# Kernel tuning notes

Hardware: AMD Instinct MI355X
Metric: run time of the kernel (lower is better)

## Reference

```python
import jax, jax.numpy as jnp
import numpy as np

N, D1, D2, B = 8, 2048, 1024, 512
D = D1 * D2
MAXBW = 3
NUM_PART = 5          # num_possible_partitions
TEMP = 0.01           # TEMPERATURE used in df_lt
DENOS = (3.0, 5.0, 17.0)  # 2^2-1, 2^2+1, 2^4+1


def ste_floor(x):
    # straight-through floor: forward floor, backward identity
    return x + jax.lax.stop_gradient(jnp.floor(x) - x)


def segmented_mean(piece, scheme, msp):
    """Replicates the inner python scan over sorted rows.
    piece:  (N, D) sorted residual errors
    scheme: (N-1, D) rounded split decisions (0/1), per column
    msp:    (N-1, D) soft split probabilities (grad factors), per column
    Returns (N, D): each row gets grad_ * (segment mean) of its segment.
    """
    n = piece.shape[0]
    buf = jnp.zeros_like(piece[0])
    cnt = jnp.zeros_like(piece[0])
    g = jnp.ones_like(piece[0])
    reset = jnp.zeros(piece.shape[1], dtype=bool)
    vlist, blist = [], []
    for i in range(n):
        buf = jnp.where(reset, piece[i], buf + piece[i])
        cnt = jnp.where(reset, 1.0, cnt + 1.0)
        g = jnp.where(reset, 1.0, g)
        if i == n - 1:
            vlist.append(g * (buf / cnt))
            blist.append(jnp.ones_like(reset))
        else:
            b = scheme[i] > 0.5
            vlist.append(jnp.where(b, g * msp[i], 0.0) * (buf / cnt))
            blist.append(b)
            g = jnp.where(b, g, g * (1.0 - msp[i]))
            reset = b
    # broadcast each segment-end value back to all rows of its segment
    out = vlist[-1]
    outs = [out]
    for i in range(n - 2, -1, -1):
        out = jnp.where(blist[i], vlist[i], out)
        outs.append(out)
    return jnp.stack(outs[::-1], axis=0)


def residual_quant(U, vsum, s, thr):
    """One residual quantization level (the update_partition=True branch)."""
    res = U - vsum                                   # (N, D)
    idx_maps = jnp.argsort(res, axis=0)              # torch.sort ascending, dim=0
    sorted_err = jnp.take_along_axis(res, idx_maps, axis=0)
    delta = sorted_err[1:] - sorted_err[:-1]         # (N-1, D), >= 0
    delta = delta / jnp.max(delta)
    msp = jax.nn.sigmoid((delta - thr) / TEMP)       # mean_split_point (N-1, D)
    rs = jnp.round(msp)                              # round_split, 0/1

    nm1 = N - 1
    P = 2 ** nm1  # all possible split-column patterns (torch.unique over dim=1)
    weights = (2 ** jnp.arange(nm1 - 1, -1, -1)).astype(jnp.int32)  # row 0 = MSB (lexicographic)
    code = jnp.sum(rs.astype(jnp.int32) * weights[:, None], axis=0)  # (D,)
    counts = jnp.zeros((P,), jnp.int32).at[code].add(1)
    present = counts > 0
    # torch.unique sorts patterns lexicographically -> rank = #present codes below
    rank_of_code = jnp.cumsum(present.astype(jnp.int32)) - present.astype(jnp.int32)
    order = jnp.argsort(-counts)                     # codes by count descending
    top_codes = order[:NUM_PART]
    top_ranks = rank_of_code[top_codes]              # s_indices[:NUM_PART]
    # binary patterns for every possible code
    patterns = ((jnp.arange(P)[:, None] >> jnp.arange(nm1 - 1, -1, -1)[None, :]) & 1).astype(jnp.float32)  # (P, N-1)
    inter = patterns @ patterns[top_codes].T         # (P, NUM_PART)
    sel = jnp.argmax(inter, axis=1)
    reassigned = top_ranks[sel]                      # (P,)
    is_top = jnp.any(rank_of_code[:, None] == top_ranks[None, :], axis=1)
    final_rank = jnp.where(is_top, rank_of_code, reassigned)  # (P,)
    c_rank = final_rank[code]                        # clustered_indices, (D,)

    # NOTE: original indexes round_split / mean_split_point columns BY the
    # unique-cluster index value s_idx (a quirk of the source); replicate it.
    scheme_used = rs[:, c_rank]                      # (N-1, D)
    msp_used = msp[:, c_rank]                        # (N-1, D)

    inner = segmented_mean(sorted_err, scheme_used, msp_used)  # (N, D)
    # einsum('cb,cba->ab', inner, one_hot(idx_maps)) == unsort along dim 0
    inv = jnp.argsort(idx_maps, axis=0)
    grouped = jnp.take_along_axis(inner, inv, axis=0)
    return s * ste_floor(grouped / s)


def setup_inputs():
    key = jax.random.key(0)
    k1, k2 = jax.random.split(key)
    x = jax.random.normal(k1, (B, N, D1), dtype=jnp.float32)
    # kaiming_normal_ on (N, D): std = sqrt(2 / fan_in), fan_in = D
    U = jax.random.normal(k2, (N, D), dtype=jnp.float32) * np.float32(np.sqrt(2.0 / D))
    thres_mean = jnp.full((D2,), -1.3, dtype=jnp.float32)
    return {"x": x, "U": U, "thres_mean": thres_mean}


def reference(x, U, thres_mean):
    beta = jnp.max(U)
    alpha = jnp.min(U)
    s = (beta - alpha) / DENOS[0]
    vsum = s * ste_floor(U / s)                      # base quantization level
    thr = jax.nn.sigmoid(jnp.repeat(thres_mean, D1))  # thres_mean.repeat_interleave(D1)
    for deno in DENOS[1:MAXBW]:
        s = s / deno
        vsum = vsum + residual_quant(U, vsum, s, thr)
    w = vsum.reshape(N, D1, D2)
    return jnp.einsum('bnd,ndl->bnl', x, w)
```

## Files before the change

### kernel.cpp

```cpp
#include <hip/hip_runtime.h>
#include <hip/hip_bf16.h>
#include <math.h>

#define NROW 8
#define DT   2097152
#define DD1  2048
#define DD2  1024
#define BATCH 512
#define NBLK 2048
#define NCH  4


typedef __attribute__((ext_vector_type(8))) short short8;
typedef __attribute__((ext_vector_type(4))) float f32x4;

__device__ __forceinline__ unsigned fenc(float f){
  unsigned u = __float_as_uint(f);
  return (u & 0x80000000u) ? ~u : (u | 0x80000000u);
}
__device__ __forceinline__ float fdec(unsigned k){
  return (k & 0x80000000u) ? __uint_as_float(k ^ 0x80000000u) : __uint_as_float(~k);
}
__device__ __forceinline__ float sigmoid_ref(float z){
  #pragma clang fp contract(off)
  return 1.0f / (1.0f + expf(-z));
}
__device__ __forceinline__ unsigned short f2bf(float f){
  __hip_bfloat16 h = __float2bfloat16(f);
  return *reinterpret_cast<unsigned short*>(&h);
}

#define CSWAPV(a,b) { float _lo=fminf(a,b), _hi=fmaxf(a,b); a=_lo; b=_hi; }
__device__ __forceinline__ void sort8v(float v[8]){
  CSWAPV(v[0],v[1]) CSWAPV(v[2],v[3]) CSWAPV(v[4],v[5]) CSWAPV(v[6],v[7])
  CSWAPV(v[0],v[2]) CSWAPV(v[1],v[3]) CSWAPV(v[4],v[6]) CSWAPV(v[5],v[7])
  CSWAPV(v[1],v[2]) CSWAPV(v[5],v[6])
  CSWAPV(v[0],v[4]) CSWAPV(v[1],v[5]) CSWAPV(v[2],v[6]) CSWAPV(v[3],v[7])
  CSWAPV(v[2],v[4]) CSWAPV(v[3],v[5])
  CSWAPV(v[1],v[2]) CSWAPV(v[3],v[4]) CSWAPV(v[5],v[6])
}
__device__ __forceinline__ void cswapkv(float&av,int&ai,float&bv,int&bi){
  bool sw = (av > bv) || ((av == bv) && (ai > bi));
  float nav = sw ? bv : av; float nbv = sw ? av : bv;
  int   nai = sw ? bi : ai; int   nbi = sw ? ai : bi;
  av = nav; bv = nbv; ai = nai; bi = nbi;
}
#define CSWAPK(i,j) cswapkv(v[i],ix[i],v[j],ix[j]);
__device__ __forceinline__ void sort8kv(float v[8], int ix[8]){
  CSWAPK(0,1) CSWAPK(2,3) CSWAPK(4,5) CSWAPK(6,7)
  CSWAPK(0,2) CSWAPK(1,3) CSWAPK(4,6) CSWAPK(5,7)
  CSWAPK(1,2) CSWAPK(5,6)
  CSWAPK(0,4) CSWAPK(1,5) CSWAPK(2,6) CSWAPK(3,7)
  CSWAPK(2,4) CSWAPK(3,5)
  CSWAPK(1,2) CSWAPK(3,4) CSWAPK(5,6)
}

__global__ void k_init(unsigned* __restrict__ meta){
  int t = threadIdx.x;
  if (t == 0){ meta[0] = 0u; meta[1] = 0xFFFFFFFFu; meta[2] = 0u; meta[3] = 0u; }
  if (t < 128){ meta[4+t] = 0u; meta[132+t] = 0u; }
}

__global__ __launch_bounds__(256) void k_minmax(const float* __restrict__ U, unsigned* __restrict__ meta){
  __shared__ unsigned smx[256], smn[256];
  int t = threadIdx.x;
  size_t i = (size_t)blockIdx.x*256 + t;
  size_t stride = (size_t)gridDim.x*256;
  float mx = -INFINITY, mn = INFINITY;
  for (; i < (size_t)NROW*DT; i += stride){ float v = U[i]; mx = fmaxf(mx,v); mn = fminf(mn,v); }
  smx[t] = fenc(mx); smn[t] = fenc(mn);
  __syncthreads();
  for (int o = 128; o > 0; o >>= 1){
    if (t < o){ smx[t] = max(smx[t], smx[t+o]); smn[t] = min(smn[t], smn[t+o]); }
    __syncthreads();
  }
  if (t == 0){ atomicMax(&meta[0], smx[0]); atomicMin(&meta[1], smn[0]); }
}

__global__ __launch_bounds__(256) void k_passA2(const float* __restrict__ U, unsigned* __restrict__ meta){
  #pragma clang fp contract(off)
  __shared__ unsigned sred[256];
  int t = threadIdx.x;
  float beta = fdec(meta[0]), alpha = fdec(meta[1]);
  float s1 = (beta - alpha) / 3.0f;
  unsigned dmax = 0u;
  for (int ch = 0; ch < NCH; ++ch){
    int d = (blockIdx.x + ch*NBLK)*256 + t;
    float res[8];
    #pragma unroll
    for (int i = 0; i < 8; ++i){
      float u = U[(size_t)i*DT + d];
      res[i] = u - s1*floorf(u/s1);
    }
    sort8v(res);
    float m = 0.0f;
    #pragma unroll
    for (int i = 0; i < 7; ++i) m = fmaxf(m, res[i+1] - res[i]);
    dmax = max(dmax, __float_as_uint(m));
  }
  sred[t] = dmax;
  __syncthreads();
  for (int o = 128; o > 0; o >>= 1){
    if (t < o) sred[t] = max(sred[t], sred[t+o]);
    __syncthreads();
  }
  if (t == 0) atomicMax(&meta[2], sred[0]);
}

template<int LEVEL>
__global__ __launch_bounds__(256) void k_passB(const float* __restrict__ U, const float* __restrict__ vsum,
                                               const float* __restrict__ thres_mean,
                                               unsigned char* __restrict__ code, unsigned* __restrict__ meta){
  #pragma clang fp contract(off)
  __shared__ int hist[128];
  int t = threadIdx.x;
  if (t < 128) hist[t] = 0;
  __syncthreads();
  float beta = fdec(meta[0]), alpha = fdec(meta[1]);
  float s1 = (beta - alpha) / 3.0f;
  float gmax = __uint_as_float(meta[(LEVEL==2)?2:3]);
  for (int ch = 0; ch < NCH; ++ch){
    int d = (blockIdx.x + ch*NBLK)*256 + t;
    float res[8];
    #pragma unroll
    for (int i = 0; i < 8; ++i){
      size_t off = (size_t)i*DT + d;
      float u = U[off];
      float b = (LEVEL==2) ? s1*floorf(u/s1) : vsum[off];
      res[i] = u - b;
    }
    sort8v(res);
    float thr = sigmoid_ref(thres_mean[d >> 11]);
    int c = 0;
    #pragma unroll
    for (int i = 0; i < 7; ++i){
      float dn  = (res[i+1] - res[i]) / gmax;
      float z   = (dn - thr) / 0.01f;
      float msp = sigmoid_ref(z);
      int bit = (int)rintf(msp);
      c = (c << 1) | bit;
    }
    code[d] = (unsigned char)c;
    atomicAdd(&hist[c], 1);
  }
  __syncthreads();
  if (t < 128 && hist[t] > 0) atomicAdd((int*)&meta[((LEVEL==2)?4:132) + t], hist[t]);
}

template<int LEVEL>
__global__ void k_small(const float* __restrict__ U, const float* __restrict__ vsum,
                        const float* __restrict__ thres_mean, unsigned* __restrict__ meta){
  #pragma clang fp contract(off)
  __shared__ int cs[128], rk[128], redk[128];
  __shared__ int top_code[5], top_rank[5];
  __shared__ int w0cnt;
  int c = threadIdx.x;
  cs[c] = (int)meta[((LEVEL==2)?4:132) + c];
  bool present = cs[c] > 0;
  unsigned long long bm = __ballot(present);
  int lane = c & 63;
  int r = (int)__popcll(bm & ((1ull << lane) - 1ull));
  if (c == 63) w0cnt = (int)__popcll(bm);
  __syncthreads();
  if (c >= 64) r += w0cnt;
  rk[c] = r;
  __syncthreads();
  for (int k = 0; k < 5; ++k){
    redk[c] = (cs[c] << 7) | (127 - c);
    __syncthreads();
    for (int o = 64; o > 0; o >>= 1){
      if (c < o) redk[c] = max(redk[c], redk[c+o]);
      __syncthreads();
    }
    if (c == 0){
      int best = 127 - (redk[0] & 127);
      top_code[k] = best; top_rank[k] = rk[best];
      cs[best] = -1;
    }
    __syncthreads();
  }
  int besti = -1, sel = 0;
  #pragma unroll
  for (int j = 0; j < 5; ++j){
    int inter = __popc(c & top_code[j]);
    if (inter > besti){ besti = inter; sel = j; }
  }
  bool is_top = false;
  #pragma unroll
  for (int j = 0; j < 5; ++j) is_top = is_top || (rk[c] == top_rank[j]);
  int fr = is_top ? rk[c] : top_rank[sel];
  ((int*)meta)[260 + c] = fr;
  float beta = fdec(meta[0]), alpha = fdec(meta[1]);
  float s1 = (beta - alpha) / 3.0f;
  float gmax = __uint_as_float(meta[(LEVEL==2)?2:3]);
  float res[8];
  #pragma unroll
  for (int i = 0; i < 8; ++i){
    size_t off = (size_t)i*DT + c;
    float u = U[off];
    float b = (LEVEL==2) ? s1*floorf(u/s1) : vsum[off];
    res[i] = u - b;
  }
  sort8v(res);
  float thr = sigmoid_ref(thres_mean[c >> 11]);
  unsigned bits = 0;
  float* msp_tab = (float*)&meta[388];
  #pragma unroll
  for (int i = 0; i < 7; ++i){
    float dn  = (res[i+1] - res[i]) / gmax;
    float z   = (dn - thr) / 0.01f;
    float msp = sigmoid_ref(z);
    msp_tab[c*7 + i] = msp;
    bits |= ((unsigned)(int)rintf(msp)) << i;
  }
  meta[1284 + c] = bits;
}

template<int LEVEL>
__global__ __launch_bounds__(256) void k_passD(const float* __restrict__ U, float* __restrict__ vsum,
                                               const unsigned char* __restrict__ code,
                                               unsigned* __restrict__ meta){
  #pragma clang fp contract(off)
  __shared__ int fr_s[128];
  __shared__ unsigned bits_s[128];
  __shared__ float msp_s[128*7];
  __shared__ unsigned sred[256];
  int t = threadIdx.x;
  if (t < 128){ fr_s[t] = ((int*)meta)[260 + t]; bits_s[t] = meta[1284 + t]; }
  for (int i = t; i < 128*7; i += 256) msp_s[i] = ((float*)&meta[388])[i];
  __syncthreads();
  float beta = fdec(meta[0]), alpha = fdec(meta[1]);
  float s1 = (beta - alpha) / 3.0f;
  float s2 = s1 / 5.0f;
  float s  = (LEVEL == 2) ? s2 : (s2 / 17.0f);
  unsigned dmax = 0u;
  for (int ch = 0; ch < NCH; ++ch){
    int d = (blockIdx.x + ch*NBLK)*256 + t;
    float u[8], base[8], v[8]; int ix[8];
    #pragma unroll
    for (int i = 0; i < 8; ++i){
      size_t off = (size_t)i*DT + d;
      u[i] = U[off];
      base[i] = (LEVEL==2) ? s1*floorf(u[i]/s1) : vsum[off];
      v[i] = u[i] - base[i];
      ix[i] = i;
    }
    sort8kv(v, ix);
    int cr = fr_s[code[d]];
    unsigned sb = bits_s[cr];
    float vv[8]; bool bl[8];
    float buf = 0.0f, cnt = 0.0f, g = 1.0f; bool reset = false;
    #pragma unroll
    for (int i = 0; i < 8; ++i){
      buf = reset ? v[i] : (buf + v[i]);
      cnt = reset ? 1.0f : (cnt + 1.0f);
      g   = reset ? 1.0f : g;
      float m = buf / cnt;
      if (i == 7){ vv[7] = g * m; bl[7] = true; }
      else {
        float msp = msp_s[cr*7 + i];
        bool b = ((sb >> i) & 1u) != 0u;
        vv[i] = b ? ((g * msp) * m) : 0.0f;
        bl[i] = b;
        g = b ? g : (g * (1.0f - msp));
        reset = b;
      }
    }
    float out = vv[7];
    float inner[8];
    inner[7] = out;
    for (int i = 6; i >= 0; --i){ if (bl[i]) out = vv[i]; inner[i] = out; }
    float res3[8];
    #pragma unroll
    for (int rr = 0; rr < 8; ++rr){
      float innr = inner[0];
      #pragma unroll
      for (int i = 1; i < 8; ++i) if (ix[i] == rr) innr = inner[i];
      if (ix[0] != rr && ix[1] != rr && ix[2] != rr && ix[3] != rr &&
          ix[4] != rr && ix[5] != rr && ix[6] != rr && ix[7] != rr) innr = inner[0];
      if (ix[0] == rr) innr = inner[0];
      float vnew = base[rr] + s * floorf(innr / s);
      vsum[(size_t)rr*DT + d] = vnew;
      if (LEVEL == 2) res3[rr] = u[rr] - vnew;
    }
    if (LEVEL == 2){
      sort8v(res3);
      float m = 0.0f;
      #pragma unroll
      for (int i = 0; i < 7; ++i) m = fmaxf(m, res3[i+1] - res3[i]);
      dmax = max(dmax, __float_as_uint(m));
    }
  }
  if (LEVEL == 2){
    sred[t] = dmax;
    __syncthreads();
    for (int o = 128; o > 0; o >>= 1){
      if (t < o) sred[t] = max(sred[t], sred[t+o]);
      __syncthreads();
    }
    if (t == 0) atomicMax(&meta[3], sred[0]);
  }
}

__global__ __launch_bounds__(256) void k_wt(const float* __restrict__ vsum, unsigned short* __restrict__ wt){
  __shared__ unsigned short tile[64][68];
  int t = threadIdx.x;
  int c = t & 63, r0 = t >> 6;
  int n = blockIdx.z, k0 = blockIdx.y*64, l0 = blockIdx.x*64;
  const float* src = vsum + (size_t)n*DT;
  #pragma unroll
  for (int i = 0; i < 16; ++i){
    int r = r0 + i*4;
    tile[r][c] = f2bf(src[(size_t)(k0+r)*DD2 + l0 + c]);
  }
  __syncthreads();
  unsigned short* dst = wt + (size_t)n*DT;
  #pragma unroll
  for (int i = 0; i < 16; ++i){
    int r = r0 + i*4;
    dst[(size_t)(l0+r)*DD1 + k0 + c] = tile[c][r];
  }
}

__global__ __launch_bounds__(256) void k_gemm(const float* __restrict__ x,
                                              const unsigned short* __restrict__ wt,
                                              float* __restrict__ out){
  __shared__ __align__(16) unsigned short As[128][72];
  __shared__ __align__(16) unsigned short Bs[128][72];
  int t = threadIdx.x;
  int lane = t & 63, wv = t >> 6;
  int n  = blockIdx.z;
  int b0 = blockIdx.y * 128;
  int l0 = blockIdx.x * 128;
  int wm = (wv >> 1) * 64, wn = (wv & 1) * 64;
  f32x4 acc[4][4] = {};
  const unsigned short* wtn = wt + (size_t)n*DT;
  int col = lane & 15, quad = lane >> 4;
  for (int k0 = 0; k0 < DD1; k0 += 64){
    #pragma unroll
    for (int i = 0; i < 8; ++i){
      int cc = t + i*256;
      int row = cc >> 4, seg = cc & 15;
      float4 a = *(const float4*)(x + (((size_t)(b0+row)*NROW + n)*DD1 + k0 + seg*4));
      ushort4 h;
      h.x = f2bf(a.x); h.y = f2bf(a.y); h.z = f2bf(a.z); h.w = f2bf(a.w);
      *(ushort4*)&As[row][seg*4] = h;
    }
    #pragma unroll
    for (int i = 0; i < 4; ++i){
      int cc = t + i*256;
      int row = cc >> 3, seg = cc & 7;
      uint4 b = *(const uint4*)(wtn + (size_t)(l0+row)*DD1 + k0 + seg*8);
      *(uint4*)&Bs[row][seg*8] = b;
    }
    __syncthreads();
    #pragma unroll
    for (int ks = 0; ks < 2; ++ks){
      int kq = ks*32 + quad*8;
      short8 af[4], bfr[4];
      #pragma unroll
      for (int mi = 0; mi < 4; ++mi) af[mi]  = *(const short8*)&As[wm + mi*16 + col][kq];
      #pragma unroll
      for (int ni = 0; ni < 4; ++ni) bfr[ni] = *(const short8*)&Bs[wn + ni*16 + col][kq];
      #pragma unroll
      for (int mi = 0; mi < 4; ++mi)
        #pragma unroll
        for (int ni = 0; ni < 4; ++ni)
          acc[mi][ni] = __builtin_amdgcn_mfma_f32_16x16x32_bf16(af[mi], bfr[ni], acc[mi][ni], 0, 0, 0);
    }
    __syncthreads();
  }
  #pragma unroll
  for (int mi = 0; mi < 4; ++mi)
    #pragma unroll
    for (int ni = 0; ni < 4; ++ni)
      #pragma unroll
      for (int r = 0; r < 4; ++r){
        int b = b0 + wm + mi*16 + quad*4 + r;
        int l = l0 + wn + ni*16 + col;
        out[((size_t)b*NROW + n)*DD2 + l] = acc[mi][ni][r];
      }
}

extern "C" void kernel_launch(void* const* d_in, const int* in_sizes, int n_in,
                              void* d_out, int out_size, void* d_ws, size_t ws_size,
                              hipStream_t stream){
  const float* x  = (const float*)d_in[0];
  const float* U  = (const float*)d_in[1];
  const float* tm = (const float*)d_in[2];
  float* out  = (float*)d_out;
  float* vsum = (float*)d_ws;
  unsigned char* code = (unsigned char*)d_ws + (size_t)NROW*DT*4;
  unsigned short* wt  = (unsigned short*)((unsigned char*)d_ws + (size_t)NROW*DT*4 + DT);
  unsigned* meta = (unsigned*)((unsigned char*)d_ws + (size_t)NROW*DT*4 + DT + (size_t)NROW*DT*2);
  (void)in_sizes; (void)n_in; (void)out_size; (void)ws_size;

  k_init  <<<1,    256, 0, stream>>>(meta);
  k_minmax<<<2048, 256, 0, stream>>>(U, meta);

  k_passA2  <<<NBLK, 256, 0, stream>>>(U, meta);
  k_passB<2><<<NBLK, 256, 0, stream>>>(U, vsum, tm, code, meta);
  k_small<2><<<1,   128, 0, stream>>>(U, vsum, tm, meta);
  k_passD<2><<<NBLK, 256, 0, stream>>>(U, vsum, code, meta);

  k_passB<3><<<NBLK, 256, 0, stream>>>(U, vsum, tm, code, meta);
  k_small<3><<<1,   128, 0, stream>>>(U, vsum, tm, meta);
  k_passD<3><<<NBLK, 256, 0, stream>>>(U, vsum, code, meta);

  k_wt  <<<dim3(DD2/64, DD1/64, NROW), 256, 0, stream>>>(vsum, wt);
  k_gemm<<<dim3(DD2/128, BATCH/128, NROW), 256, 0, stream>>>(x, wt, out);
}
```

Measured before the change: 477.0 us.

## Vectorize quantization passes, pre-cast x to bf16, use async LDS loads in GEMM

The minmax, passA2, passB and passD kernels now load U/vsum as float4/float2 per thread, each thread handling 4 or 2 contiguous columns, with code bytes and vsum stored as vectors. passD uses twice as many blocks. The transpose kernel reads float4 and writes ushort4. A new kernel converts x to bf16 up front, reusing the vsum workspace. The GEMM then fills unpadded LDS with global_load_lds 16-byte async copies and uses 64x128 tiles. The goal is fewer, wider memory transactions and cheaper GEMM staging, at the cost of an extra pass over x and possible LDS bank conflicts from dropping the padding.

After: 475.9 us. No clear change (-0.2%).

```diff
diff --git a/kernel.cpp b/kernel.cpp
--- a/kernel.cpp
+++ b/kernel.cpp
@@ -7,8 +7,8 @@
 #define DD1  2048
 #define DD2  1024
 #define BATCH 512
-#define NBLK 2048
-#define NCH  4
+#define NBLK4 2048
+#define NBLK2 4096
 
 
 typedef __attribute__((ext_vector_type(8))) short short8;
@@ -28,6 +28,10 @@
 __device__ __forceinline__ unsigned short f2bf(float f){
   __hip_bfloat16 h = __float2bfloat16(f);
   return *reinterpret_cast<unsigned short*>(&h);
+}
+__device__ __forceinline__ void async16(const unsigned short* g, unsigned short* l){
+  __builtin_amdgcn_global_load_lds((const __attribute__((address_space(1))) unsigned int*)g,
+                                   (__attribute__((address_space(3))) unsigned int*)l, 16, 0, 0);
 }
 
 #define CSWAPV(a,b) { float _lo=fminf(a,b), _hi=fmaxf(a,b); a=_lo; b=_hi; }
@@ -66,8 +70,13 @@
   int t = threadIdx.x;
   size_t i = (size_t)blockIdx.x*256 + t;
   size_t stride = (size_t)gridDim.x*256;
+  const float4* U4 = (const float4*)U;
   float mx = -INFINITY, mn = INFINITY;
-  for (; i < (size_t)NROW*DT; i += stride){ float v = U[i]; mx = fmaxf(mx,v); mn = fminf(mn,v); }
+  for (; i < (size_t)NROW*DT/4; i += stride){
+    float4 v = U4[i];
+    mx = fmaxf(fmaxf(mx,v.x), fmaxf(v.y, fmaxf(v.z,v.w)));
+    mn = fminf(fminf(mn,v.x), fminf(v.y, fminf(v.z,v.w)));
+  }
   smx[t] = fenc(mx); smn[t] = fenc(mn);
   __syncthreads();
   for (int o = 128; o > 0; o >>= 1){
@@ -81,16 +90,20 @@
   #pragma clang fp contract(off)
   __shared__ unsigned sred[256];
   int t = threadIdx.x;
+  int d0 = (blockIdx.x*256 + t)*4;
   float beta = fdec(meta[0]), alpha = fdec(meta[1]);
   float s1 = (beta - alpha) / 3.0f;
+  float4 u[8];
+  #pragma unroll
+  for (int i = 0; i < 8; ++i) u[i] = *(const float4*)(U + (size_t)i*DT + d0);
   unsigned dmax = 0u;
-  for (int ch = 0; ch < NCH; ++ch){
-    int d = (blockIdx.x + ch*NBLK)*256 + t;
+  #pragma unroll
+  for (int c = 0; c < 4; ++c){
     float res[8];
     #pragma unroll
     for (int i = 0; i < 8; ++i){
-      float u = U[(size_t)i*DT + d];
-      res[i] = u - s1*floorf(u/s1);
+      float uv = ((const float*)&u[i])[c];
+      res[i] = uv - s1*floorf(uv/s1);
     }
     sort8v(res);
     float m = 0.0f;
@@ -116,33 +129,45 @@
   int t = threadIdx.x;
   if (t < 128) hist[t] = 0;
   __syncthreads();
+  int d0 = (blockIdx.x*256 + t)*4;
   float beta = fdec(meta[0]), alpha = fdec(meta[1]);
   float s1 = (beta - alpha) / 3.0f;
   float gmax = __uint_as_float(meta[(LEVEL==2)?2:3]);
-  for (int ch = 0; ch < NCH; ++ch){
-    int d = (blockIdx.x + ch*NBLK)*256 + t;
+  float4 u[8], b[8];
+  #pragma unroll
+  for (int i = 0; i < 8; ++i){
+    u[i] = *(const float4*)(U + (size_t)i*DT + d0);
+    if (LEVEL == 2){
+      float4 bb;
+      bb.x = s1*floorf(u[i].x/s1); bb.y = s1*floorf(u[i].y/s1);
+      bb.z = s1*floorf(u[i].z/s1); bb.w = s1*floorf(u[i].w/s1);
+      b[i] = bb;
+    } else {
+      b[i] = *(const float4*)(vsum + (size_t)i*DT + d0);
+    }
+  }
+  float thr = sigmoid_ref(thres_mean[d0 >> 11]);
+  uchar4 cods;
+  unsigned char* cp = (unsigned char*)&cods;
+  #pragma unroll
+  for (int c = 0; c < 4; ++c){
     float res[8];
     #pragma unroll
-    for (int i = 0; i < 8; ++i){
-      size_t off = (size_t)i*DT + d;
-      float u = U[off];
-      float b = (LEVEL==2) ? s1*floorf(u/s1) : vsum[off];
-      res[i] = u - b;
-    }
+    for (int i = 0; i < 8; ++i) res[i] = ((const float*)&u[i])[c] - ((const float*)&b[i])[c];
     sort8v(res);
-    float thr = sigmoid_ref(thres_mean[d >> 11]);
-    int c = 0;
+    int cd = 0;
     #pragma unroll
     for (int i = 0; i < 7; ++i){
       float dn  = (res[i+1] - res[i]) / gmax;
       float z   = (dn - thr) / 0.01f;
       float msp = sigmoid_ref(z);
       int bit = (int)rintf(msp);
-      c = (c << 1) | bit;
-    }
-    code[d] = (unsigned char)c;
-    atomicAdd(&hist[c], 1);
-  }
+      cd = (cd << 1) | bit;
+    }
+    cp[c] = (unsigned char)cd;
+    atomicAdd(&hist[cd], 1);
+  }
+  *(uchar4*)(code + d0) = cods;
   __syncthreads();
   if (t < 128 && hist[t] > 0) atomicAdd((int*)&meta[((LEVEL==2)?4:132) + t], hist[t]);
 }
@@ -229,24 +254,36 @@
   if (t < 128){ fr_s[t] = ((int*)meta)[260 + t]; bits_s[t] = meta[1284 + t]; }
   for (int i = t; i < 128*7; i += 256) msp_s[i] = ((float*)&meta[388])[i];
   __syncthreads();
+  int d0 = (blockIdx.x*256 + t)*2;
   float beta = fdec(meta[0]), alpha = fdec(meta[1]);
   float s1 = (beta - alpha) / 3.0f;
   float s2 = s1 / 5.0f;
   float s  = (LEVEL == 2) ? s2 : (s2 / 17.0f);
+  float2 u2[8], b2[8];
+  #pragma unroll
+  for (int i = 0; i < 8; ++i){
+    u2[i] = *(const float2*)(U + (size_t)i*DT + d0);
+    if (LEVEL == 2){
+      b2[i].x = s1*floorf(u2[i].x/s1);
+      b2[i].y = s1*floorf(u2[i].y/s1);
+    } else {
+      b2[i] = *(const float2*)(vsum + (size_t)i*DT + d0);
+    }
+  }
+  unsigned char cd2[2];
+  *(ushort*)cd2 = *(const ushort*)(code + d0);
+  float vnew[2][8];
   unsigned dmax = 0u;
-  for (int ch = 0; ch < NCH; ++ch){
-    int d = (blockIdx.x + ch*NBLK)*256 + t;
-    float u[8], base[8], v[8]; int ix[8];
+  #pragma unroll
+  for (int c = 0; c < 2; ++c){
+    float v[8]; int ix[8];
     #pragma unroll
     for (int i = 0; i < 8; ++i){
-      size_t off = (size_t)i*DT + d;
-      u[i] = U[off];
-      base[i] = (LEVEL==2) ? s1*floorf(u[i]/s1) : vsum[off];
-      v[i] = u[i] - base[i];
+      v[i] = ((const float*)&u2[i])[c] - ((const float*)&b2[i])[c];
       ix[i] = i;
     }
     sort8kv(v, ix);
-    int cr = fr_s[code[d]];
+    int cr = fr_s[cd2[c]];
     unsigned sb = bits_s[cr];
     float vv[8]; bool bl[8];
     float buf = 0.0f, cnt = 0.0f, g = 1.0f; bool reset = false;
@@ -275,13 +312,10 @@
     for (int rr = 0; rr < 8; ++rr){
       float innr = inner[0];
       #pragma unroll
-      for (int i = 1; i < 8; ++i) if (ix[i] == rr) innr = inner[i];
-      if (ix[0] != rr && ix[1] != rr && ix[2] != rr && ix[3] != rr &&
-          ix[4] != rr && ix[5] != rr && ix[6] != rr && ix[7] != rr) innr = inner[0];
-      if (ix[0] == rr) innr = inner[0];
-      float vnew = base[rr] + s * floorf(innr / s);
-      vsum[(size_t)rr*DT + d] = vnew;
-      if (LEVEL == 2) res3[rr] = u[rr] - vnew;
+      for (int i = 0; i < 8; ++i) innr = (ix[i] == rr) ? inner[i] : innr;
+      float vn = ((const float*)&b2[rr])[c] + s * floorf(innr / s);
+      vnew[c][rr] = vn;
+      if (LEVEL == 2) res3[rr] = ((const float*)&u2[rr])[c] - vn;
     }
     if (LEVEL == 2){
       sort8v(res3);
@@ -291,6 +325,11 @@
       dmax = max(dmax, __float_as_uint(m));
     }
   }
+  #pragma unroll
+  for (int rr = 0; rr < 8; ++rr){
+    float2 o; o.x = vnew[0][rr]; o.y = vnew[1][rr];
+    *(float2*)(vsum + (size_t)rr*DT + d0) = o;
+  }
   if (LEVEL == 2){
     sred[t] = dmax;
     __syncthreads();
@@ -305,65 +344,75 @@
 __global__ __launch_bounds__(256) void k_wt(const float* __restrict__ vsum, unsigned short* __restrict__ wt){
   __shared__ unsigned short tile[64][68];
   int t = threadIdx.x;
-  int c = t & 63, r0 = t >> 6;
+  int c4 = t & 15, r0 = t >> 4;
   int n = blockIdx.z, k0 = blockIdx.y*64, l0 = blockIdx.x*64;
   const float* src = vsum + (size_t)n*DT;
   #pragma unroll
-  for (int i = 0; i < 16; ++i){
-    int r = r0 + i*4;
-    tile[r][c] = f2bf(src[(size_t)(k0+r)*DD2 + l0 + c]);
+  for (int i = 0; i < 4; ++i){
+    int r = r0 + i*16;
+    float4 v = *(const float4*)(src + (size_t)(k0+r)*DD2 + l0 + c4*4);
+    tile[r][c4*4+0] = f2bf(v.x); tile[r][c4*4+1] = f2bf(v.y);
+    tile[r][c4*4+2] = f2bf(v.z); tile[r][c4*4+3] = f2bf(v.w);
   }
   __syncthreads();
   unsigned short* dst = wt + (size_t)n*DT;
   #pragma unroll
-  for (int i = 0; i < 16; ++i){
-    int r = r0 + i*4;
-    dst[(size_t)(l0+r)*DD1 + k0 + c] = tile[c][r];
-  }
-}
-
-__global__ __launch_bounds__(256) void k_gemm(const float* __restrict__ x,
+  for (int i = 0; i < 4; ++i){
+    int rl = r0 + i*16;
+    ushort4 o;
+    o.x = tile[c4*4+0][rl]; o.y = tile[c4*4+1][rl];
+    o.z = tile[c4*4+2][rl]; o.w = tile[c4*4+3][rl];
+    *(ushort4*)(dst + (size_t)(l0+rl)*DD1 + k0 + c4*4) = o;
+  }
+}
+
+__global__ __launch_bounds__(256) void k_xb(const float* __restrict__ x, unsigned short* __restrict__ xb){
+  int idx = (blockIdx.x*256 + threadIdx.x)*4;
+  float4 v = *(const float4*)(x + idx);
+  ushort4 o;
+  o.x = f2bf(v.x); o.y = f2bf(v.y); o.z = f2bf(v.z); o.w = f2bf(v.w);
+  *(ushort4*)(xb + idx) = o;
+}
+
+__global__ __launch_bounds__(256) void k_gemm(const unsigned short* __restrict__ xb,
                                               const unsigned short* __restrict__ wt,
                                               float* __restrict__ out){
-  __shared__ __align__(16) unsigned short As[128][72];
-  __shared__ __align__(16) unsigned short Bs[128][72];
+  __shared__ __align__(16) unsigned short As[64*64];
+  __shared__ __align__(16) unsigned short Bs[128*64];
   int t = threadIdx.x;
   int lane = t & 63, wv = t >> 6;
   int n  = blockIdx.z;
-  int b0 = blockIdx.y * 128;
+  int b0 = blockIdx.y * 64;
   int l0 = blockIdx.x * 128;
-  int wm = (wv >> 1) * 64, wn = (wv & 1) * 64;
-  f32x4 acc[4][4] = {};
+  int wm = (wv >> 1) * 32, wn = (wv & 1) * 64;
+  int col = lane & 15, quad = lane >> 4;
+  int arow = lane >> 3, aseg = lane & 7;
   const unsigned short* wtn = wt + (size_t)n*DT;
-  int col = lane & 15, quad = lane >> 4;
+  f32x4 acc[2][4] = {};
   for (int k0 = 0; k0 < DD1; k0 += 64){
     #pragma unroll
-    for (int i = 0; i < 8; ++i){
-      int cc = t + i*256;
-      int row = cc >> 4, seg = cc & 15;
-      float4 a = *(const float4*)(x + (((size_t)(b0+row)*NROW + n)*DD1 + k0 + seg*4));
-      ushort4 h;
-      h.x = f2bf(a.x); h.y = f2bf(a.y); h.z = f2bf(a.z); h.w = f2bf(a.w);
-      *(ushort4*)&As[row][seg*4] = h;
+    for (int i = 0; i < 2; ++i){
+      int row = wv*16 + i*8 + arow;
+      const unsigned short* g = xb + (((size_t)(b0+row)*NROW + n)*DD1 + k0 + aseg*8);
+      async16(g, &As[(wv*16 + i*8)*64]);
     }
     #pragma unroll
     for (int i = 0; i < 4; ++i){
-      int cc = t + i*256;
-      int row = cc >> 3, seg = cc & 7;
-      uint4 b = *(const uint4*)(wtn + (size_t)(l0+row)*DD1 + k0 + seg*8);
-      *(uint4*)&Bs[row][seg*8] = b;
+      int row = wv*32 + i*8 + arow;
+      const unsigned short* g = wtn + ((size_t)(l0+row)*DD1 + k0 + aseg*8);
+      async16(g, &Bs[(wv*32 + i*8)*64]);
     }
     __syncthreads();
     #pragma unroll
     for (int ks = 0; ks < 2; ++ks){
       int kq = ks*32 + quad*8;
-      short8 af[4], bfr[4];
-      #pragma unroll
-      for (int mi = 0; mi < 4; ++mi) af[mi]  = *(const short8*)&As[wm + mi*16 + col][kq];
-      #pragma unroll
-      for (int ni = 0; ni < 4; ++ni) bfr[ni] = *(const short8*)&Bs[wn + ni*16 + col][kq];
-      #pragma unroll
-      for (int mi = 0; mi < 4; ++mi)
+      short8 af[2], bfr[4];
+      #pragma unroll
+      for (int mi = 0; mi < 2; ++mi) af[mi]  = *(const short8*)&As[(wm + mi*16 + col)*64 + kq];
+      #pragma unroll
+      for (int ni = 0; ni < 4; ++ni) bfr[ni] = *(const short8*)&Bs[(wn + ni*16 + col)*64 + kq];
+      #pragma unroll
+      for (int mi = 0; mi < 2; ++mi)
         #pragma unroll
         for (int ni = 0; ni < 4; ++ni)
           acc[mi][ni] = __builtin_amdgcn_mfma_f32_16x16x32_bf16(af[mi], bfr[ni], acc[mi][ni], 0, 0, 0);
@@ -371,7 +420,7 @@
     __syncthreads();
   }
   #pragma unroll
-  for (int mi = 0; mi < 4; ++mi)
+  for (int mi = 0; mi < 2; ++mi)
     #pragma unroll
     for (int ni = 0; ni < 4; ++ni)
       #pragma unroll
@@ -393,20 +442,22 @@
   unsigned char* code = (unsigned char*)d_ws + (size_t)NROW*DT*4;
   unsigned short* wt  = (unsigned short*)((unsigned char*)d_ws + (size_t)NROW*DT*4 + DT);
   unsigned* meta = (unsigned*)((unsigned char*)d_ws + (size_t)NROW*DT*4 + DT + (size_t)NROW*DT*2);
+  unsigned short* xb = (unsigned short*)d_ws;
   (void)in_sizes; (void)n_in; (void)out_size; (void)ws_size;
 
   k_init  <<<1,    256, 0, stream>>>(meta);
   k_minmax<<<2048, 256, 0, stream>>>(U, meta);
 
-  k_passA2  <<<NBLK, 256, 0, stream>>>(U, meta);
-  k_passB<2><<<NBLK, 256, 0, stream>>>(U, vsum, tm, code, meta);
-  k_small<2><<<1,   128, 0, stream>>>(U, vsum, tm, meta);
-  k_passD<2><<<NBLK, 256, 0, stream>>>(U, vsum, code, meta);
-
-  k_passB<3><<<NBLK, 256, 0, stream>>>(U, vsum, tm, code, meta);
-  k_small<3><<<1,   128, 0, stream>>>(U, vsum, tm, meta);
-  k_passD<3><<<NBLK, 256, 0, stream>>>(U, vsum, code, meta);
+  k_passA2  <<<NBLK4, 256, 0, stream>>>(U, meta);
+  k_passB<2><<<NBLK4, 256, 0, stream>>>(U, vsum, tm, code, meta);
+  k_small<2><<<1,    128, 0, stream>>>(U, vsum, tm, meta);
+  k_passD<2><<<NBLK2, 256, 0, stream>>>(U, vsum, code, meta);
+
+  k_passB<3><<<NBLK4, 256, 0, stream>>>(U, vsum, tm, code, meta);
+  k_small<3><<<1,    128, 0, stream>>>(U, vsum, tm, meta);
+  k_passD<3><<<NBLK2, 256, 0, stream>>>(U, vsum, code, meta);
 
   k_wt  <<<dim3(DD2/64, DD1/64, NROW), 256, 0, stream>>>(vsum, wt);
-  k_gemm<<<dim3(DD2/128, BATCH/128, NROW), 256, 0, stream>>>(x, wt, out);
-}
+  k_xb  <<<(BATCH*NROW*DD1)/1024, 256, 0, stream>>>(x, xb);
+  k_gemm<<<dim3(DD2/128, BATCH/64, NROW), 256, 0, stream>>>(xb, wt, out);
+}
```
